# Performance work log

Hardware: AMD Instinct MI355X
Metric: run time of the kernel (lower is better)

The kernel has to match this reference:

```python
import jax, jax.numpy as jnp
import numpy as np

# static graph structure: B graphs, each with NPER nodes and DEG*NPER edges
B = 128        # graphs in batch
NPER = 400     # nodes per graph (fMRI atlas ROIs)
DEG = 16       # avg degree
EPG = NPER * DEG
E = B * EPG    # 819200 edges total
F_IN = 400     # num_features
H = 128        # hidden dim of GraphConv
C = 2          # num_classes
K1, K2, K3 = 320, 256, 205  # ceil(0.8*400), ceil(0.8*320), ceil(0.8*256)


def setup_inputs() -> dict:
    key = jax.random.key(0)
    ks = jax.random.split(key, 24)
    x = jax.random.normal(ks[0], (B * NPER, F_IN), dtype=jnp.float32)
    # edges constrained within each graph (PyG batched disjoint-union convention)
    src_l = jax.random.randint(ks[1], (B, EPG), 0, NPER)
    dst_l = jax.random.randint(ks[2], (B, EPG), 0, NPER)
    off = (jnp.arange(B, dtype=jnp.int32) * NPER)[:, None]
    edge_src = (src_l + off).reshape(-1).astype(jnp.int32)
    edge_dst = (dst_l + off).reshape(-1).astype(jnp.int32)
    batch = jnp.repeat(jnp.arange(B, dtype=jnp.int32), NPER)
    s = 0.05
    p = {
        'Wrel1': jax.random.normal(ks[3], (H, F_IN)) * s,
        'Wroot1': jax.random.normal(ks[4], (H, F_IN)) * s,
        'b1': jnp.zeros((H,), jnp.float32),
        'pw1': jax.random.normal(ks[5], (H,)) * s,
        'Wrel2': jax.random.normal(ks[6], (H, H)) * s,
        'Wroot2': jax.random.normal(ks[7], (H, H)) * s,
        'b2': jnp.zeros((H,), jnp.float32),
        'pw2': jax.random.normal(ks[8], (H,)) * s,
        'Wrel3': jax.random.normal(ks[9], (H, H)) * s,
        'Wroot3': jax.random.normal(ks[10], (H, H)) * s,
        'b3': jnp.zeros((H,), jnp.float32),
        'pw3': jax.random.normal(ks[11], (H,)) * s,
        'W1': jax.random.normal(ks[12], (128, 256)) * s,
        'bl1': jnp.zeros((128,), jnp.float32),
        'W2': jax.random.normal(ks[13], (64, 128)) * s,
        'bl2': jnp.zeros((64,), jnp.float32),
        'W3': jax.random.normal(ks[14], (C, 64)) * s,
        'bl3': jnp.zeros((C,), jnp.float32),
    }
    return dict(x=x, edge_src=edge_src, edge_dst=edge_dst, batch=batch, **p)


def _graph_conv(x, src, dst, emask, Wrel, b, Wroot):
    # PyG GraphConv: lin_rel(sum_j x_j) + lin_root(x_i); masked edges contribute 0
    msg = x[src] * emask[:, None]
    agg = jax.ops.segment_sum(msg, dst, num_segments=x.shape[0])
    return agg @ Wrel.T + b + x @ Wroot.T


def _topk_pool(x, src, dst, emask, w, npg, k):
    # score = x.w / ||w||; keep top-k per graph; gate kept x by tanh(score)
    score = (x @ w) / (jnp.linalg.norm(w) + 1e-16)
    vals, idx = jax.lax.top_k(score.reshape(B, npg), k)      # [B,k]
    perm = (jnp.arange(B, dtype=jnp.int32)[:, None] * npg + idx).reshape(-1)
    xk = x[perm] * jnp.tanh(vals).reshape(-1)[:, None]
    new_id = jnp.full((B * npg,), -1, jnp.int32).at[perm].set(
        jnp.arange(B * k, dtype=jnp.int32))
    ns, nd = new_id[src], new_id[dst]
    keep = (ns >= 0) & (nd >= 0)
    em2 = emask * keep.astype(emask.dtype)
    return xk, jnp.where(keep, ns, 0), jnp.where(keep, nd, 0), em2


def _readout(x, k):
    xr = x.reshape(B, k, H)
    return jnp.concatenate([xr.max(axis=1), xr.mean(axis=1)], axis=1)  # [B,256]


def reference(x, edge_src, edge_dst, batch,
              Wrel1, Wroot1, b1, pw1, Wrel2, Wroot2, b2, pw2,
              Wrel3, Wroot3, b3, pw3, W1, bl1, W2, bl2, W3, bl3):
    em = jnp.ones((E,), jnp.float32)
    h = jax.nn.relu(_graph_conv(x, edge_src, edge_dst, em, Wrel1, b1, Wroot1))
    h, s, d, em = _topk_pool(h, edge_src, edge_dst, em, pw1, NPER, K1)
    x1 = _readout(h, K1)
    h = jax.nn.relu(_graph_conv(h, s, d, em, Wrel2, b2, Wroot2))
    h, s, d, em = _topk_pool(h, s, d, em, pw2, K1, K2)
    x2 = _readout(h, K2)
    h = jax.nn.relu(_graph_conv(h, s, d, em, Wrel3, b3, Wroot3))
    h, s, d, em = _topk_pool(h, s, d, em, pw3, K2, K3)
    x3 = _readout(h, K3)
    z = x1 + x2 + x3
    z = jax.nn.relu(z @ W1.T + bl1)  # dropout is identity in eval mode
    z = jax.nn.relu(z @ W2.T + bl2)
    return jax.nn.log_softmax(z @ W3.T + bl3, axis=-1)
```

## Files before the change

kernel.cpp:

```cpp
#include <hip/hip_runtime.h>
#include <math.h>

#define BATCH 128
#define NPER 400
#define EPG 6400
#define NEDGE 819200
#define F_IN 400
#define HD 128
#define K1 320
#define K2 256
#define K3 205

typedef __bf16 bf16x8 __attribute__((ext_vector_type(8)));
typedef float f32x4 __attribute__((ext_vector_type(4)));

__device__ __forceinline__ unsigned short f2bf(float f) {
    unsigned u = __builtin_bit_cast(unsigned, f);
    unsigned r = u + 0x7fffu + ((u >> 16) & 1u);
    return (unsigned short)(r >> 16);
}
__device__ __forceinline__ float bf2f(unsigned short s) {
    unsigned u = ((unsigned)s) << 16;
    return __builtin_bit_cast(float, u);
}

static constexpr size_t SZ_TREL = 51200ull * 128 * 4;
static constexpr size_t OFF_TREL = 0;
static constexpr size_t OFF_H    = OFF_TREL + SZ_TREL;
static constexpr size_t OFF_HP   = OFF_H + SZ_TREL;
static constexpr size_t OFF_SC   = OFF_HP + 40960ull * 128 * 4;
static constexpr size_t OFF_ES   = OFF_SC + 51200ull * 4;
static constexpr size_t OFF_ED   = OFF_ES + (size_t)NEDGE * 4;
static constexpr size_t OFF_EM   = OFF_ED + (size_t)NEDGE * 4;
static constexpr size_t OFF_Z    = OFF_EM + (size_t)NEDGE * 4;
static constexpr size_t OFF_COFF = OFF_Z + 128ull * 256 * 4;
static constexpr size_t OFF_CDEG = OFF_COFF + 51200ull * 4;
static constexpr size_t OFF_CSRC = OFF_CDEG + 51200ull * 4;
static constexpr size_t OFF_W1H  = OFF_CSRC + (size_t)NEDGE * 4;
static constexpr size_t OFF_W1L  = OFF_W1H + 16ull * 13 * 512 * 2;
static constexpr size_t OFF_W2H  = OFF_W1L + 16ull * 13 * 512 * 2;
static constexpr size_t OFF_W2L  = OFF_W2H + 16ull * 4 * 512 * 2;
static constexpr size_t OFF_W3H  = OFF_W2L + 16ull * 4 * 512 * 2;
static constexpr size_t OFF_W3L  = OFF_W3H + 16ull * 4 * 512 * 2;

__global__ __launch_bounds__(64) void prep_w_all(
    const float* __restrict__ Wrel1, const float* __restrict__ Wroot1,
    const float* __restrict__ Wrel2, const float* __restrict__ Wroot2,
    const float* __restrict__ Wrel3, const float* __restrict__ Wroot3,
    unsigned short* __restrict__ b1h, unsigned short* __restrict__ b1l,
    unsigned short* __restrict__ b2h, unsigned short* __restrict__ b2l,
    unsigned short* __restrict__ b3h, unsigned short* __restrict__ b3l) {
    const int layer = blockIdx.z;
    const int s = blockIdx.x;
    const int ntile = blockIdx.y;
    const int Ks = (layer == 0) ? 13 : 4;
    const int Kd = (layer == 0) ? F_IN : HD;
    if (s >= Ks) return;
    const float* Wrel  = (layer == 0) ? Wrel1  : (layer == 1) ? Wrel2  : Wrel3;
    const float* Wroot = (layer == 0) ? Wroot1 : (layer == 1) ? Wroot2 : Wroot3;
    unsigned short* bh = (layer == 0) ? b1h : (layer == 1) ? b2h : b3h;
    unsigned short* bl = (layer == 0) ? b1l : (layer == 1) ? b2l : b3l;
    const int t = threadIdx.x;
    const int rowin = t & 15, qd = t >> 4;
    const int n = ntile * 16 + rowin;
    const int k = s * 32 + qd * 8;
    const float* src = (n < 128) ? &Wrel[(n & 127) * Kd] : &Wroot[(n & 127) * Kd];
    unsigned short hv[8], lv[8];
#pragma unroll
    for (int e = 0; e < 8; e++) {
        float f = (k + e < Kd) ? src[k + e] : 0.f;
        unsigned short hi = f2bf(f);
        hv[e] = hi;
        lv[e] = f2bf(f - bf2f(hi));
    }
    size_t o = ((size_t)ntile * Ks + s) * 512 + (size_t)t * 8;
#pragma unroll
    for (int e = 0; e < 8; e++) { bh[o + e] = hv[e]; bl[o + e] = lv[e]; }
}

template <int Ks, int Kd>
__global__ __launch_bounds__(256, 3) void gemm_mfma(
    const float* __restrict__ A,
    const unsigned short* __restrict__ bh_p, const unsigned short* __restrict__ bl_p,
    float* __restrict__ t_rel, float* __restrict__ h) {
    __shared__ char Alds[2][8192];
    const int tid = threadIdx.x;
    const int lane = tid & 63;
    const int wv = tid >> 6;
    const int lm = lane & 15;
    const int qd = (lane >> 4) & 3;
    const int m0 = blockIdx.x * 64;
    const int nt0 = wv * 4;

    const int srow = tid >> 2;
    const int sqd = tid & 3;
    const int woff = ((srow >> 4) << 10) + (sqd << 8) + ((srow & 15) << 4);
    const float* Arow = A + (size_t)(m0 + srow) * Kd + sqd * 8;

    f32x4 acc[4][4];
#pragma unroll
    for (int i = 0; i < 4; i++)
#pragma unroll
        for (int j = 0; j < 4; j++) acc[i][j] = (f32x4){0.f, 0.f, 0.f, 0.f};

    auto gload = [&](int s, float4& x0, float4& x1) {
        if (s * 32 + sqd * 8 < Kd) {
            const float* p = Arow + s * 32;
            x0 = *(const float4*)p;
            x1 = *(const float4*)(p + 4);
        } else {
            x0 = make_float4(0.f, 0.f, 0.f, 0.f);
            x1 = x0;
        }
    };
    auto cvwrite = [&](int buf, const float4& x0, const float4& x1) {
        float fe[8] = {x0.x, x0.y, x0.z, x0.w, x1.x, x1.y, x1.z, x1.w};
        bf16x8 hv, lv;
#pragma unroll
        for (int e = 0; e < 8; e++) {
            __bf16 hb = (__bf16)fe[e];
            hv[e] = hb;
            lv[e] = (__bf16)(fe[e] - (float)hb);
        }
        *(bf16x8*)(&Alds[buf][woff]) = hv;
        *(bf16x8*)(&Alds[buf][4096 + woff]) = lv;
    };

    float4 r0a, r0b, r1a, r1b;
    gload(0, r0a, r0b);
    if (Ks > 1) gload(1, r1a, r1b);
    cvwrite(0, r0a, r0b);
    asm volatile("s_waitcnt lgkmcnt(0)" ::: "memory");
    __builtin_amdgcn_s_barrier();
    asm volatile("" ::: "memory");

#pragma unroll
    for (int s = 0; s < Ks; ++s) {
        bf16x8 bhc[4], blc[4];
#pragma unroll
        for (int j = 0; j < 4; j++)
            bhc[j] = *(const bf16x8*)&bh_p[((size_t)(nt0 + j) * Ks + s) * 512 + lane * 8];
#pragma unroll
        for (int j = 0; j < 4; j++)
            blc[j] = *(const bf16x8*)&bl_p[((size_t)(nt0 + j) * Ks + s) * 512 + lane * 8];

        const char* Ab = &Alds[s & 1][0];
        bf16x8 ah[4], al[4];
#pragma unroll
        for (int i = 0; i < 4; i++) {
            ah[i] = *(const bf16x8*)(Ab + i * 1024 + lane * 16);
            al[i] = *(const bf16x8*)(Ab + 4096 + i * 1024 + lane * 16);
        }

        if (s + 1 < Ks) {
            if ((s + 1) & 1) cvwrite((s + 1) & 1, r1a, r1b);
            else             cvwrite((s + 1) & 1, r0a, r0b);
        }
        if (s + 2 < Ks) {
            if ((s + 2) & 1) gload(s + 2, r1a, r1b);
            else             gload(s + 2, r0a, r0b);
        }

        __builtin_amdgcn_s_setprio(1);
#pragma unroll
        for (int j = 0; j < 4; j++)
#pragma unroll
            for (int i = 0; i < 4; i++)
                acc[i][j] = __builtin_amdgcn_mfma_f32_16x16x32_bf16(
                    ah[i], bhc[j], acc[i][j], 0, 0, 0);
#pragma unroll
        for (int j = 0; j < 4; j++)
#pragma unroll
            for (int i = 0; i < 4; i++)
                acc[i][j] = __builtin_amdgcn_mfma_f32_16x16x32_bf16(
                    al[i], bhc[j], acc[i][j], 0, 0, 0);
#pragma unroll
        for (int j = 0; j < 4; j++)
#pragma unroll
            for (int i = 0; i < 4; i++)
                acc[i][j] = __builtin_amdgcn_mfma_f32_16x16x32_bf16(
                    ah[i], blc[j], acc[i][j], 0, 0, 0);
        __builtin_amdgcn_s_setprio(0);

        asm volatile("s_waitcnt lgkmcnt(0)" ::: "memory");
        __builtin_amdgcn_s_barrier();
        asm volatile("" ::: "memory");
    }
    float* out = (wv < 2) ? t_rel : h;
    const int colbase = (wv & 1) * 64;
#pragma unroll
    for (int i = 0; i < 4; i++)
#pragma unroll
        for (int j = 0; j < 4; j++) {
            int row = m0 + i * 16 + qd * 4;
            int col = colbase + j * 16 + lm;
#pragma unroll
            for (int r = 0; r < 4; r++)
                out[(size_t)(row + r) * 128 + col] = acc[i][j][r];
        }
}

__global__ __launch_bounds__(1024) void csr_build0(
    const int* __restrict__ gsrc, const int* __restrict__ gdst,
    int* __restrict__ csr_off, int* __restrict__ csr_deg, int* __restrict__ csr_src) {
    __shared__ int cnt[NPER];
    __shared__ int cur[NPER];
    __shared__ int sscan[512];
    const int g = blockIdx.x;
    const int t = threadIdx.x;
    for (int i = t; i < NPER; i += 1024) cnt[i] = 0;
    __syncthreads();
    for (int e = t; e < EPG; e += 1024) {
        int dl = gdst[g * EPG + e] - g * NPER;
        atomicAdd(&cnt[dl], 1);
    }
    __syncthreads();
    if (t < 512) sscan[t] = (t < NPER) ? cnt[t] : 0;
    __syncthreads();
    for (int d = 1; d < 512; d <<= 1) {
        int v = 0;
        if (t < 512 && t >= d) v = sscan[t - d];
        __syncthreads();
        if (t < 512 && t >= d) sscan[t] += v;
        __syncthreads();
    }
    if (t < NPER) {
        int excl = (t == 0) ? 0 : sscan[t - 1];
        int st = g * EPG + excl;
        csr_off[g * NPER + t] = st;
        csr_deg[g * NPER + t] = cnt[t];
        cur[t] = st;
    }
    __syncthreads();
    for (int e = t; e < EPG; e += 1024) {
        int eg = g * EPG + e;
        int dl = gdst[eg] - g * NPER;
        int slot = atomicAdd(&cur[dl], 1);
        csr_src[slot] = gsrc[eg];
    }
}

__global__ __launch_bounds__(256) void agg_score(
    const float* __restrict__ t_rel,
    const int* __restrict__ csr_off, const int* __restrict__ csr_deg,
    const int* __restrict__ csr_src,
    const float* __restrict__ bias, const float* __restrict__ pw,
    float* __restrict__ h, float* __restrict__ sc, int npg) {
    const int xcd = blockIdx.x & 7;
    const int j = blockIdx.x >> 3;
    const int bpg = npg >> 2;
    const int graph = xcd * (BATCH / 8) + j / bpg;
    const int nblk = j - (j / bpg) * bpg;
    const int wid = graph * npg + nblk * 4 + (threadIdx.x >> 6);
    const int lane = threadIdx.x & 63;

    const int start = csr_off[wid];
    const int deg = csr_deg[wid];
    const size_t fo = (size_t)lane * 2;
    float a0 = 0.f, a1 = 0.f, b0 = 0.f, b1 = 0.f;
    float c0 = 0.f, c1 = 0.f, d0 = 0.f, d1 = 0.f;
    int e = 0;
    for (; e + 4 <= deg; e += 4) {
        int s0 = csr_src[start + e];
        int s1 = csr_src[start + e + 1];
        int s2 = csr_src[start + e + 2];
        int s3 = csr_src[start + e + 3];
        float2 v0 = *(const float2*)&t_rel[(size_t)s0 * 128 + fo];
        float2 v1 = *(const float2*)&t_rel[(size_t)s1 * 128 + fo];
        float2 v2 = *(const float2*)&t_rel[(size_t)s2 * 128 + fo];
        float2 v3 = *(const float2*)&t_rel[(size_t)s3 * 128 + fo];
        a0 += v0.x; a1 += v0.y;
        b0 += v1.x; b1 += v1.y;
        c0 += v2.x; c1 += v2.y;
        d0 += v3.x; d1 += v3.y;
    }
    for (; e < deg; e++) {
        int s0 = csr_src[start + e];
        float2 v0 = *(const float2*)&t_rel[(size_t)s0 * 128 + fo];
        a0 += v0.x; a1 += v0.y;
    }
    a0 += b0 + c0 + d0;
    a1 += b1 + c1 + d1;

    float2 bb = *(const float2*)&bias[fo];
    size_t o = (size_t)wid * 128 + fo;
    float2 hv = *(const float2*)&h[o];
    hv.x = fmaxf(hv.x + a0 + bb.x, 0.f);
    hv.y = fmaxf(hv.y + a1 + bb.y, 0.f);
    *(float2*)&h[o] = hv;
    float2 pp = *(const float2*)&pw[fo];
    float d = hv.x * pp.x + hv.y * pp.y;
    float nr = pp.x * pp.x + pp.y * pp.y;
#pragma unroll
    for (int off = 32; off; off >>= 1) {
        d += __shfl_down(d, off, 64);
        nr += __shfl_down(nr, off, 64);
    }
    if (lane == 0) sc[wid] = d / (sqrtf(nr) + 1e-16f);
}

__global__ __launch_bounds__(1024) void topk_pool(
    const float* __restrict__ sc, const float* __restrict__ h,
    float* __restrict__ hp, float* __restrict__ z,
    const int* __restrict__ gsrc, const int* __restrict__ gdst,
    int* __restrict__ es, int* __restrict__ ed, int* __restrict__ em,
    int* __restrict__ csr_off, int* __restrict__ csr_deg, int* __restrict__ csr_src,
    int npg, int k, int mode) {
    __shared__ float svals[NPER];
    __shared__ int si[512];
    __shared__ int nid[NPER];
    __shared__ float tgs[K1];
    __shared__ int packed[EPG];
    __shared__ int cnt[K1];
    __shared__ int cur[K1];
    __shared__ int sscan[512];
    __shared__ float pmx[8][128], psm[8][128];
    const int g = blockIdx.x;
    const int t = threadIdx.x;

    for (int i = t; i < npg; i += 1024) svals[i] = sc[g * npg + i];
    if (t < K1) cnt[t] = 0;
    __syncthreads();
    if (t < npg) {
        const float mine = svals[t];
        int r = 0;
        for (int j4 = 0; j4 < npg; j4 += 4) {
            float4 v = *(const float4*)&svals[j4];
            r += (v.x > mine) ? 1 : ((v.x == mine) & (j4 + 0 < t)) ? 1 : 0;
            r += (v.y > mine) ? 1 : ((v.y == mine) & (j4 + 1 < t)) ? 1 : 0;
            r += (v.z > mine) ? 1 : ((v.z == mine) & (j4 + 2 < t)) ? 1 : 0;
            r += (v.w > mine) ? 1 : ((v.w == mine) & (j4 + 3 < t)) ? 1 : 0;
        }
        nid[t] = (r < k) ? r : -1;
        if (r < k) {
            si[r] = t;
            tgs[r] = tanhf(mine);
        }
    }
    __syncthreads();

    {
        const int f = t & 127;
        const int jq = t >> 7;
        float mx = -INFINITY, sm = 0.f;
        for (int j = jq; j < k; j += 8) {
            float v = h[(size_t)(g * npg + si[j]) * 128 + f] * tgs[j];
            if (mode != 2) hp[(size_t)(g * k + j) * 128 + f] = v;
            mx = fmaxf(mx, v);
            sm += v;
        }
        pmx[jq][f] = mx; psm[jq][f] = sm;
        __syncthreads();
        if (t < 128) {
            mx = pmx[0][t]; sm = psm[0][t];
#pragma unroll
            for (int q = 1; q < 8; q++) {
                mx = fmaxf(mx, pmx[q][t]);
                sm += psm[q][t];
            }
            z[g * 256 + t] += mx;
            z[g * 256 + 128 + t] += sm / (float)k;
        }
    }
    if (mode == 2) return;

    for (int e = t; e < EPG; e += 1024) {
        int eg = g * EPG + e;
        int sl, dl, m;
        if (mode == 0) { sl = gsrc[eg] - g * NPER; dl = gdst[eg] - g * NPER; m = 1; }
        else           { sl = es[eg]; dl = ed[eg]; m = em[eg]; }
        int ns = nid[sl], nd = nid[dl];
        int keep = (m && ns >= 0 && nd >= 0) ? 1 : 0;
        es[eg] = keep ? ns : 0;
        ed[eg] = keep ? nd : 0;
        em[eg] = keep;
        packed[e] = keep ? (ns | (nd << 16)) : -1;
        if (keep) atomicAdd(&cnt[nd], 1);
    }
    __syncthreads();
    if (t < 512) sscan[t] = (t < k) ? cnt[t] : 0;
    __syncthreads();
    for (int d = 1; d < 512; d <<= 1) {
        int v = 0;
        if (t < 512 && t >= d) v = sscan[t - d];
        __syncthreads();
        if (t < 512 && t >= d) sscan[t] += v;
        __syncthreads();
    }
    if (t < k) {
        int excl = (t == 0) ? 0 : sscan[t - 1];
        int st = g * EPG + excl;
        csr_off[g * k + t] = st;
        csr_deg[g * k + t] = cnt[t];
        cur[t] = st;
    }
    __syncthreads();
    for (int e = t; e < EPG; e += 1024) {
        int p = packed[e];
        if (p >= 0) {
            int ns = p & 0xffff, nd = p >> 16;
            int slot = atomicAdd(&cur[nd], 1);
            csr_src[slot] = g * k + ns;
        }
    }
}

__global__ __launch_bounds__(256) void mlp_head(const float* __restrict__ z,
                                                const float* __restrict__ W1,
                                                const float* __restrict__ bl1,
                                                const float* __restrict__ W2,
                                                const float* __restrict__ bl2,
                                                const float* __restrict__ W3,
                                                const float* __restrict__ bl3,
                                                float* __restrict__ out) {
    __shared__ float zs[256], l1[128], l2[64];
    const int g = blockIdx.x, t = threadIdx.x;
    zs[t] = z[g * 256 + t];
    __syncthreads();
    if (t < 128) {
        float s = bl1[t];
        const float* w = &W1[t * 256];
        for (int i = 0; i < 256; i++) s += w[i] * zs[i];
        l1[t] = fmaxf(s, 0.f);
    }
    __syncthreads();
    if (t < 64) {
        float s = bl2[t];
        const float* w = &W2[t * 128];
        for (int i = 0; i < 128; i++) s += w[i] * l1[i];
        l2[t] = fmaxf(s, 0.f);
    }
    __syncthreads();
    if (t == 0) {
        float a = bl3[0], b = bl3[1];
        for (int i = 0; i < 64; i++) { a += W3[i] * l2[i]; b += W3[64 + i] * l2[i]; }
        float m = fmaxf(a, b);
        float lse = m + logf(expf(a - m) + expf(b - m));
        out[g * 2 + 0] = a - lse;
        out[g * 2 + 1] = b - lse;
    }
}

extern "C" void kernel_launch(void* const* d_in, const int* in_sizes, int n_in,
                              void* d_out, int out_size, void* d_ws, size_t ws_size,
                              hipStream_t stream) {
    const float* x        = (const float*)d_in[0];
    const int*   edge_src = (const int*)d_in[1];
    const int*   edge_dst = (const int*)d_in[2];
    const float* Wrel1 = (const float*)d_in[4];
    const float* Wroot1= (const float*)d_in[5];
    const float* b1    = (const float*)d_in[6];
    const float* pw1   = (const float*)d_in[7];
    const float* Wrel2 = (const float*)d_in[8];
    const float* Wroot2= (const float*)d_in[9];
    const float* b2    = (const float*)d_in[10];
    const float* pw2   = (const float*)d_in[11];
    const float* Wrel3 = (const float*)d_in[12];
    const float* Wroot3= (const float*)d_in[13];
    const float* b3    = (const float*)d_in[14];
    const float* pw3   = (const float*)d_in[15];
    const float* W1    = (const float*)d_in[16];
    const float* bl1   = (const float*)d_in[17];
    const float* W2    = (const float*)d_in[18];
    const float* bl2   = (const float*)d_in[19];
    const float* W3    = (const float*)d_in[20];
    const float* bl3   = (const float*)d_in[21];

    char* ws = (char*)d_ws;
    float* t_rel = (float*)(ws + OFF_TREL);
    float* h     = (float*)(ws + OFF_H);
    float* hp    = (float*)(ws + OFF_HP);
    float* sc    = (float*)(ws + OFF_SC);
    int*   es    = (int*)(ws + OFF_ES);
    int*   ed    = (int*)(ws + OFF_ED);
    int*   em    = (int*)(ws + OFF_EM);
    float* z     = (float*)(ws + OFF_Z);
    int*   coff  = (int*)(ws + OFF_COFF);
    int*   cdeg  = (int*)(ws + OFF_CDEG);
    int*   csrc  = (int*)(ws + OFF_CSRC);
    unsigned short* w1h = (unsigned short*)(ws + OFF_W1H);
    unsigned short* w1l = (unsigned short*)(ws + OFF_W1L);
    unsigned short* w2h = (unsigned short*)(ws + OFF_W2H);
    unsigned short* w2l = (unsigned short*)(ws + OFF_W2L);
    unsigned short* w3h = (unsigned short*)(ws + OFF_W3H);
    unsigned short* w3l = (unsigned short*)(ws + OFF_W3L);

    hipMemsetAsync(z, 0, 128ull * 256 * 4, stream);
    prep_w_all<<<dim3(13, 16, 3), 64, 0, stream>>>(
        Wrel1, Wroot1, Wrel2, Wroot2, Wrel3, Wroot3,
        w1h, w1l, w2h, w2l, w3h, w3l);
    csr_build0<<<BATCH, 1024, 0, stream>>>(edge_src, edge_dst, coff, cdeg, csrc);

    gemm_mfma<13, F_IN><<<800, 256, 0, stream>>>(x, w1h, w1l, t_rel, h);
    agg_score<<<51200 / 4, 256, 0, stream>>>(t_rel, coff, cdeg, csrc, b1, pw1,
                                             h, sc, NPER);
    topk_pool<<<BATCH, 1024, 0, stream>>>(sc, h, hp, z, edge_src, edge_dst,
                                          es, ed, em, coff, cdeg, csrc,
                                          NPER, K1, 0);

    gemm_mfma<4, HD><<<640, 256, 0, stream>>>(hp, w2h, w2l, t_rel, h);
    agg_score<<<40960 / 4, 256, 0, stream>>>(t_rel, coff, cdeg, csrc, b2, pw2,
                                             h, sc, K1);
    topk_pool<<<BATCH, 1024, 0, stream>>>(sc, h, hp, z, nullptr, nullptr,
                                          es, ed, em, coff, cdeg, csrc,
                                          K1, K2, 1);

    gemm_mfma<4, HD><<<512, 256, 0, stream>>>(hp, w3h, w3l, t_rel, h);
    agg_score<<<32768 / 4, 256, 0, stream>>>(t_rel, coff, cdeg, csrc, b3, pw3,
                                             h, sc, K2);
    topk_pool<<<BATCH, 1024, 0, stream>>>(sc, h, nullptr, z, nullptr, nullptr,
                                          es, ed, em, coff, cdeg, csrc,
                                          K2, K3, 2);

    mlp_head<<<BATCH, 256, 0, stream>>>(z, W1, bl1, W2, bl2, W3, bl3, (float*)d_out);
}
```

Baseline: 438.8 us.

## Pack edge state, widen aggregation loads, parallelize MLP head

Three separate changes. The aggregation kernel now assigns each node to a half-wavefront of 32 lanes using 16-byte loads, so a 256-thread block handles 8 nodes instead of 4. The topk pool merges the three per-edge arrays (src, dst, mask) into one packed 32-bit word with 10-bit fields, cutting per-edge global reads and writes from three to one. The MLP head spreads its first two layers over all 256 threads with shuffle reductions, and its final layer over 64 lanes, replacing the old serial single-thread loop.

```diff
diff --git a/kernel.cpp b/kernel.cpp
--- a/kernel.cpp
+++ b/kernel.cpp
@@ -29,10 +29,8 @@
 static constexpr size_t OFF_H    = OFF_TREL + SZ_TREL;
 static constexpr size_t OFF_HP   = OFF_H + SZ_TREL;
 static constexpr size_t OFF_SC   = OFF_HP + 40960ull * 128 * 4;
-static constexpr size_t OFF_ES   = OFF_SC + 51200ull * 4;
-static constexpr size_t OFF_ED   = OFF_ES + (size_t)NEDGE * 4;
-static constexpr size_t OFF_EM   = OFF_ED + (size_t)NEDGE * 4;
-static constexpr size_t OFF_Z    = OFF_EM + (size_t)NEDGE * 4;
+static constexpr size_t OFF_EPK  = OFF_SC + 51200ull * 4;
+static constexpr size_t OFF_Z    = OFF_EPK + (size_t)NEDGE * 4 * 3;
 static constexpr size_t OFF_COFF = OFF_Z + 128ull * 256 * 4;
 static constexpr size_t OFF_CDEG = OFF_COFF + 51200ull * 4;
 static constexpr size_t OFF_CSRC = OFF_CDEG + 51200ull * 4;
@@ -248,53 +246,49 @@
     float* __restrict__ h, float* __restrict__ sc, int npg) {
     const int xcd = blockIdx.x & 7;
     const int j = blockIdx.x >> 3;
-    const int bpg = npg >> 2;
+    const int bpg = npg >> 3;
     const int graph = xcd * (BATCH / 8) + j / bpg;
     const int nblk = j - (j / bpg) * bpg;
-    const int wid = graph * npg + nblk * 4 + (threadIdx.x >> 6);
-    const int lane = threadIdx.x & 63;
+    const int hw = threadIdx.x >> 5;
+    const int lane = threadIdx.x & 31;
+    const int wid = graph * npg + nblk * 8 + hw;
 
     const int start = csr_off[wid];
     const int deg = csr_deg[wid];
-    const size_t fo = (size_t)lane * 2;
-    float a0 = 0.f, a1 = 0.f, b0 = 0.f, b1 = 0.f;
-    float c0 = 0.f, c1 = 0.f, d0 = 0.f, d1 = 0.f;
+    const size_t fo = (size_t)lane * 4;
+    f32x4 a = {0.f, 0.f, 0.f, 0.f}, b = a, c = a, d4 = a;
     int e = 0;
     for (; e + 4 <= deg; e += 4) {
         int s0 = csr_src[start + e];
         int s1 = csr_src[start + e + 1];
         int s2 = csr_src[start + e + 2];
         int s3 = csr_src[start + e + 3];
-        float2 v0 = *(const float2*)&t_rel[(size_t)s0 * 128 + fo];
-        float2 v1 = *(const float2*)&t_rel[(size_t)s1 * 128 + fo];
-        float2 v2 = *(const float2*)&t_rel[(size_t)s2 * 128 + fo];
-        float2 v3 = *(const float2*)&t_rel[(size_t)s3 * 128 + fo];
-        a0 += v0.x; a1 += v0.y;
-        b0 += v1.x; b1 += v1.y;
-        c0 += v2.x; c1 += v2.y;
-        d0 += v3.x; d1 += v3.y;
+        f32x4 v0 = *(const f32x4*)&t_rel[(size_t)s0 * 128 + fo];
+        f32x4 v1 = *(const f32x4*)&t_rel[(size_t)s1 * 128 + fo];
+        f32x4 v2 = *(const f32x4*)&t_rel[(size_t)s2 * 128 + fo];
+        f32x4 v3 = *(const f32x4*)&t_rel[(size_t)s3 * 128 + fo];
+        a += v0; b += v1; c += v2; d4 += v3;
     }
     for (; e < deg; e++) {
         int s0 = csr_src[start + e];
-        float2 v0 = *(const float2*)&t_rel[(size_t)s0 * 128 + fo];
-        a0 += v0.x; a1 += v0.y;
-    }
-    a0 += b0 + c0 + d0;
-    a1 += b1 + c1 + d1;
-
-    float2 bb = *(const float2*)&bias[fo];
+        f32x4 v0 = *(const f32x4*)&t_rel[(size_t)s0 * 128 + fo];
+        a += v0;
+    }
+    a += b + c + d4;
+
+    f32x4 bb = *(const f32x4*)&bias[fo];
     size_t o = (size_t)wid * 128 + fo;
-    float2 hv = *(const float2*)&h[o];
-    hv.x = fmaxf(hv.x + a0 + bb.x, 0.f);
-    hv.y = fmaxf(hv.y + a1 + bb.y, 0.f);
-    *(float2*)&h[o] = hv;
-    float2 pp = *(const float2*)&pw[fo];
-    float d = hv.x * pp.x + hv.y * pp.y;
-    float nr = pp.x * pp.x + pp.y * pp.y;
-#pragma unroll
-    for (int off = 32; off; off >>= 1) {
-        d += __shfl_down(d, off, 64);
-        nr += __shfl_down(nr, off, 64);
+    f32x4 hv = *(const f32x4*)&h[o];
+#pragma unroll
+    for (int q = 0; q < 4; q++) hv[q] = fmaxf(hv[q] + a[q] + bb[q], 0.f);
+    *(f32x4*)&h[o] = hv;
+    f32x4 pp = *(const f32x4*)&pw[fo];
+    float d = hv[0] * pp[0] + hv[1] * pp[1] + hv[2] * pp[2] + hv[3] * pp[3];
+    float nr = pp[0] * pp[0] + pp[1] * pp[1] + pp[2] * pp[2] + pp[3] * pp[3];
+#pragma unroll
+    for (int off = 16; off; off >>= 1) {
+        d += __shfl_down(d, off, 32);
+        nr += __shfl_down(nr, off, 32);
     }
     if (lane == 0) sc[wid] = d / (sqrtf(nr) + 1e-16f);
 }
@@ -303,7 +297,7 @@
     const float* __restrict__ sc, const float* __restrict__ h,
     float* __restrict__ hp, float* __restrict__ z,
     const int* __restrict__ gsrc, const int* __restrict__ gdst,
-    int* __restrict__ es, int* __restrict__ ed, int* __restrict__ em,
+    int* __restrict__ epk,
     int* __restrict__ csr_off, int* __restrict__ csr_deg, int* __restrict__ csr_src,
     int npg, int k, int mode) {
     __shared__ float svals[NPER];
@@ -368,12 +362,10 @@
         int eg = g * EPG + e;
         int sl, dl, m;
         if (mode == 0) { sl = gsrc[eg] - g * NPER; dl = gdst[eg] - g * NPER; m = 1; }
-        else           { sl = es[eg]; dl = ed[eg]; m = em[eg]; }
+        else           { int p = epk[eg]; sl = p & 1023; dl = (p >> 10) & 1023; m = p >> 20; }
         int ns = nid[sl], nd = nid[dl];
         int keep = (m && ns >= 0 && nd >= 0) ? 1 : 0;
-        es[eg] = keep ? ns : 0;
-        ed[eg] = keep ? nd : 0;
-        em[eg] = keep;
+        epk[eg] = keep ? (ns | (nd << 10) | (1 << 20)) : 0;
         packed[e] = keep ? (ns | (nd << 16)) : -1;
         if (keep) atomicAdd(&cnt[nd], 1);
     }
@@ -417,27 +409,42 @@
     const int g = blockIdx.x, t = threadIdx.x;
     zs[t] = z[g * 256 + t];
     __syncthreads();
-    if (t < 128) {
-        float s = bl1[t];
-        const float* w = &W1[t * 256];
-        for (int i = 0; i < 256; i++) s += w[i] * zs[i];
-        l1[t] = fmaxf(s, 0.f);
+    {
+        const int o = t >> 1, half = t & 1;
+        const float* w = &W1[o * 256 + half * 128];
+        const float* zp = &zs[half * 128];
+        float s = 0.f;
+        for (int i = 0; i < 128; i++) s += w[i] * zp[i];
+        s += __shfl_down(s, 1, 64);
+        if (half == 0) l1[o] = fmaxf(s + bl1[o], 0.f);
+    }
+    __syncthreads();
+    {
+        const int o = t >> 2, q = t & 3;
+        const float* w = &W2[o * 128 + q * 32];
+        const float* lp = &l1[q * 32];
+        float s = 0.f;
+        for (int i = 0; i < 32; i++) s += w[i] * lp[i];
+        s += __shfl_down(s, 2, 64);
+        s += __shfl_down(s, 1, 64);
+        if (q == 0) l2[o] = fmaxf(s + bl2[o], 0.f);
     }
     __syncthreads();
     if (t < 64) {
-        float s = bl2[t];
-        const float* w = &W2[t * 128];
-        for (int i = 0; i < 128; i++) s += w[i] * l1[i];
-        l2[t] = fmaxf(s, 0.f);
-    }
-    __syncthreads();
-    if (t == 0) {
-        float a = bl3[0], b = bl3[1];
-        for (int i = 0; i < 64; i++) { a += W3[i] * l2[i]; b += W3[64 + i] * l2[i]; }
-        float m = fmaxf(a, b);
-        float lse = m + logf(expf(a - m) + expf(b - m));
-        out[g * 2 + 0] = a - lse;
-        out[g * 2 + 1] = b - lse;
+        float pa = W3[t] * l2[t];
+        float pb = W3[64 + t] * l2[t];
+#pragma unroll
+        for (int off = 32; off; off >>= 1) {
+            pa += __shfl_down(pa, off, 64);
+            pb += __shfl_down(pb, off, 64);
+        }
+        if (t == 0) {
+            float A = pa + bl3[0], B = pb + bl3[1];
+            float m = fmaxf(A, B);
+            float lse = m + logf(expf(A - m) + expf(B - m));
+            out[g * 2 + 0] = A - lse;
+            out[g * 2 + 1] = B - lse;
+        }
     }
 }
 
@@ -471,9 +478,7 @@
     float* h     = (float*)(ws + OFF_H);
     float* hp    = (float*)(ws + OFF_HP);
     float* sc    = (float*)(ws + OFF_SC);
-    int*   es    = (int*)(ws + OFF_ES);
-    int*   ed    = (int*)(ws + OFF_ED);
-    int*   em    = (int*)(ws + OFF_EM);
+    int*   epk   = (int*)(ws + OFF_EPK);
     float* z     = (float*)(ws + OFF_Z);
     int*   coff  = (int*)(ws + OFF_COFF);
     int*   cdeg  = (int*)(ws + OFF_CDEG);
@@ -492,24 +497,24 @@
     csr_build0<<<BATCH, 1024, 0, stream>>>(edge_src, edge_dst, coff, cdeg, csrc);
 
     gemm_mfma<13, F_IN><<<800, 256, 0, stream>>>(x, w1h, w1l, t_rel, h);
-    agg_score<<<51200 / 4, 256, 0, stream>>>(t_rel, coff, cdeg, csrc, b1, pw1,
+    agg_score<<<51200 / 8, 256, 0, stream>>>(t_rel, coff, cdeg, csrc, b1, pw1,
                                              h, sc, NPER);
     topk_pool<<<BATCH, 1024, 0, stream>>>(sc, h, hp, z, edge_src, edge_dst,
-                                          es, ed, em, coff, cdeg, csrc,
+                                          epk, coff, cdeg, csrc,
                                           NPER, K1, 0);
 
     gemm_mfma<4, HD><<<640, 256, 0, stream>>>(hp, w2h, w2l, t_rel, h);
-    agg_score<<<40960 / 4, 256, 0, stream>>>(t_rel, coff, cdeg, csrc, b2, pw2,
+    agg_score<<<40960 / 8, 256, 0, stream>>>(t_rel, coff, cdeg, csrc, b2, pw2,
                                              h, sc, K1);
     topk_pool<<<BATCH, 1024, 0, stream>>>(sc, h, hp, z, nullptr, nullptr,
-                                          es, ed, em, coff, cdeg, csrc,
+                                          epk, coff, cdeg, csrc,
                                           K1, K2, 1);
 
     gemm_mfma<4, HD><<<512, 256, 0, stream>>>(hp, w3h, w3l, t_rel, h);
-    agg_score<<<32768 / 4, 256, 0, stream>>>(t_rel, coff, cdeg, csrc, b3, pw3,
+    agg_score<<<32768 / 8, 256, 0, stream>>>(t_rel, coff, cdeg, csrc, b3, pw3,
                                              h, sc, K2);
     topk_pool<<<BATCH, 1024, 0, stream>>>(sc, h, nullptr, z, nullptr, nullptr,
-                                          es, ed, em, coff, cdeg, csrc,
+                                          epk, coff, cdeg, csrc,
                                           K2, K3, 2);
 
     mlp_head<<<BATCH, 256, 0, stream>>>(z, W1, bl1, W2, bl2, W3, bl3, (float*)d_out);
```

Result: faster. 401.7 us (-8.5%).
